# Kernel optimization log

Measured on AMD Instinct MI355X. Metric: run time of the kernel, lower is better.

Reference implementation:

```python
import jax, jax.numpy as jnp
import numpy as np

B, C, H, W = 16, 256, 64, 64
OUT_C = 3
N_TOKENS = 512
N_RES = 3
RED = 4
CB = C // RED  # bottleneck channels in ResChain
DN = ('NCHW', 'OIHW', 'NCHW')


def _conv(x, w, pad):
    return jax.lax.conv_general_dilated(x, w, (1, 1), pad, dimension_numbers=DN)


def setup_inputs() -> dict:
    key = jax.random.key(0)
    ks = jax.random.split(key, 8)
    return {
        'input': jax.random.normal(ks[0], (B, C, H, W), jnp.float32),
        'embed': jax.random.normal(ks[1], (C, N_TOKENS), jnp.float32),  # Quantize codebook [dim, n_embed]
        'res_w1': jax.random.normal(ks[2], (N_RES, CB, C, 3, 3), jnp.float32) * 0.02,
        'res_b1': jnp.zeros((N_RES, CB), jnp.float32),
        'res_w2': jax.random.normal(ks[3], (N_RES, C, CB, 1, 1), jnp.float32) * 0.02,
        'res_b2': jnp.zeros((N_RES, C), jnp.float32),
        'out_w': jax.random.normal(ks[4], (OUT_C, C, 1, 1), jnp.float32) * 0.02,
        'out_b': jnp.zeros((OUT_C,), jnp.float32),
    }


def reference(input, embed, res_w1, res_b1, res_w2, res_b2, out_w, out_b):
    sg = jax.lax.stop_gradient
    # --- Quantize (VQ-VAE codebook lookup, straight-through) ---
    x = jnp.transpose(input, (0, 2, 3, 1))  # [B,H,W,C]
    flat = x.reshape(-1, C)                  # [N, C]
    # squared L2 distance to each code: ||f||^2 - 2 f.e + ||e||^2
    dist = (flat * flat).sum(-1, keepdims=True) - 2.0 * (flat @ embed) + (embed * embed).sum(0)
    idx = jnp.argmin(dist, axis=-1).reshape(B, H, W)        # [B,H,W] int
    quantize = jnp.take(embed.T, idx, axis=0)               # embed_code: [B,H,W,C]
    diff = jnp.mean((sg(quantize) - x) ** 2)
    quantize = x + sg(quantize - x)                         # straight-through
    q = jnp.transpose(quantize, (0, 3, 1, 2))               # [B,C,H,W]
    # --- dec: ResChain(n_res_block) + 1x1 conv ---
    for i in range(N_RES):
        h = jax.nn.relu(q)
        h = _conv(h, res_w1[i], 'SAME') + res_b1[i][None, :, None, None]
        h = jax.nn.relu(h)
        h = _conv(h, res_w2[i], 'VALID') + res_b2[i][None, :, None, None]
        q = q + h
    quant = _conv(q, out_w, 'VALID') + out_b[None, :, None, None]  # [B,OUT_C,H,W]
    # --- wordfreq: per-batch bincount over idx (no grad) ---
    flat_idx = idx.reshape(B, -1)
    seg = (flat_idx + jnp.arange(B, dtype=flat_idx.dtype)[:, None] * N_TOKENS).reshape(-1)
    counts = jax.ops.segment_sum(jnp.ones_like(seg, jnp.float32), seg, num_segments=B * N_TOKENS)
    wordfreq = counts.reshape(B, N_TOKENS) / float(H * W)
    return quant, diff.reshape(1), wordfreq
```

## Files before the change

### kernel.cpp

```cpp
#include <hip/hip_runtime.h>


typedef __attribute__((ext_vector_type(8))) short short8;
typedef __attribute__((ext_vector_type(16))) float f32x16;
typedef __attribute__((ext_vector_type(8))) _Float16 half8;
typedef __attribute__((ext_vector_type(2))) _Float16 half2_t;
typedef unsigned short ushort_t;
typedef unsigned long long u64;

#define WS_QA    0
#define WS_QB    8388608
#define WS_ET    16777216
#define WS_EN    16842752
#define WS_EPK   16843264
#define WS_W1PK  16908800
#define WS_W2PK  17129984
#define WS_DIFF  17154560
#define WS_TOK   17154568
#define WS_DST   17220104
#define WS_FN    17285640
#define WS_WL    17351176

#define MARGIN 0.12f

__device__ inline ushort_t f2bf(float f) {
  unsigned u = __float_as_uint(f);
  return (ushort_t)((u + 0x7fffu + ((u >> 16) & 1u)) >> 16);
}
__device__ inline float bf2f(ushort_t h) { return __uint_as_float(((unsigned)h) << 16); }
union HU { _Float16 h; ushort_t u; };
union S8H { short8 s; half8 h; half2_t h2[4]; };

__global__ __launch_bounds__(256) void prep_kernel(
    const float* __restrict__ embed, const float* __restrict__ w1,
    const float* __restrict__ w2, float* __restrict__ ws, float* __restrict__ wf) {
  int i = blockIdx.x * 256 + threadIdx.x;
  if (i < 131072) {
    int t = i >> 8, c = i & 255;
    ((ushort_t*)(ws + WS_ET))[i] = f2bf(embed[c * 512 + t]);
  }
  if (i < 512) {
    float s = 0.f;
    for (int c = 0; c < 256; ++c) { float v = embed[c * 512 + i]; s += v * v; }
    ws[WS_EN + i] = s;
  }
  if (i < 131072) {
    int j = i & 7, lane = (i >> 3) & 63, at = (i >> 9) & 15, ks = i >> 13;
    int code = at * 32 + (lane & 31);
    int c = ks * 16 + (lane >> 5) * 8 + j;
    HU cv; cv.h = (_Float16)embed[c * 512 + code];
    ((ushort_t*)(ws + WS_EPK))[i] = cv.u;
  }
  if (i < 442368) {
    int j = i & 7; int lane = (i >> 3) & 63; int of = (i >> 9) & 1;
    int k16 = (i >> 10) & 15; int rest = i >> 14;
    int tap = rest % 9; int layer = rest / 9;
    int oc = of * 32 + (lane & 31);
    int c = k16 * 16 + (lane >> 5) * 8 + j;
    ((ushort_t*)(ws + WS_W1PK))[i] = f2bf(w1[((layer * 64 + oc) * 256 + c) * 9 + tap]);
  }
  if (i < 49152) {
    int j = i & 7, lane = (i >> 3) & 63, at = (i >> 9) & 7, ks = (i >> 12) & 3, l = i >> 14;
    int co = at * 32 + (lane & 31), cb = ks * 16 + (lane >> 5) * 8 + j;
    ((ushort_t*)(ws + WS_W2PK))[i] = f2bf(w2[(l * 256 + co) * 64 + cb]);
  }
  if (i < 8192) wf[i] = 0.f;
  if (i == 0) { ws[WS_DIFF] = 0.f; ((int*)(ws + WS_WL))[0] = 0; }
}

__global__ __launch_bounds__(512, 4) void dist_kernel(
    const float* __restrict__ input, const half8* __restrict__ epk,
    const float* __restrict__ enorm, int* __restrict__ tok,
    float* __restrict__ dst, float* __restrict__ fnv, int* __restrict__ wl) {
  __shared__ __align__(16) ushort_t sfp[2048 * 8];
  __shared__ float senorm[512];
  __shared__ float trim1[512], trim2[512];
  __shared__ int   trii[512];

  int blk = blockIdx.x, b = blk >> 6, hw0 = (blk & 63) << 6;
  int tid = threadIdx.x, lane = tid & 63, wave = tid >> 6;
  senorm[tid] = enorm[tid];

  {
    int cg = tid >> 3, sub = tid & 7;
    int ks_s = cg >> 2, hi_s = (cg >> 1) & 1, jq = cg & 1;
    const float* src0 = input + ((size_t)(b * 256 + cg * 4)) * 4096 + hw0 + sub * 8;
    float vv[4][8];
#pragma unroll
    for (int m = 0; m < 4; ++m) {
      const float4* s4 = (const float4*)(src0 + (size_t)m * 4096);
      float4 aa = s4[0], bb = s4[1];
      vv[m][0] = aa.x; vv[m][1] = aa.y; vv[m][2] = aa.z; vv[m][3] = aa.w;
      vv[m][4] = bb.x; vv[m][5] = bb.y; vv[m][6] = bb.z; vv[m][7] = bb.w;
    }
    u64* sfp64 = (u64*)sfp;
#pragma unroll
    for (int i = 0; i < 8; ++i) {
      int pl = sub * 8 + i;
      int bt = pl >> 5, lw = (pl & 31) + 32 * hi_s;
      u64 pk = 0;
#pragma unroll
      for (int m = 0; m < 4; ++m) {
        HU cv; cv.h = (_Float16)vv[m][i];
        pk |= ((u64)cv.u) << (16 * m);
      }
      sfp64[((bt * 16 + ks_s) * 64 + lw) * 2 + jq] = pk;
    }
  }
  __syncthreads();

  f32x16 acc[2][2];
#pragma unroll
  for (int bt = 0; bt < 2; ++bt)
#pragma unroll
    for (int a = 0; a < 2; ++a)
#pragma unroll
      for (int r = 0; r < 16; ++r) acc[bt][a][r] = 0.f;

  const short8* sfp8 = (const short8*)sfp;
  float fnp0 = 0.f, fnp1 = 0.f;
#pragma unroll 2
  for (int ks = 0; ks < 16; ++ks) {
    S8H u0, u1;
    u0.s = sfp8[ks * 64 + lane];
    u1.s = sfp8[(16 + ks) * 64 + lane];
#if __has_builtin(__builtin_amdgcn_fdot2)
#pragma unroll
    for (int k = 0; k < 4; ++k) {
      fnp0 = __builtin_amdgcn_fdot2(u0.h2[k], u0.h2[k], fnp0, false);
      fnp1 = __builtin_amdgcn_fdot2(u1.h2[k], u1.h2[k], fnp1, false);
    }
#else
#pragma unroll
    for (int k = 0; k < 8; ++k) {
      float v0 = (float)u0.h[k], v1 = (float)u1.h[k];
      fnp0 += v0 * v0; fnp1 += v1 * v1;
    }
#endif
#pragma unroll
    for (int a = 0; a < 2; ++a) {
      half8 ah = epk[(ks * 16 + wave * 2 + a) * 64 + lane];
      acc[0][a] = __builtin_amdgcn_mfma_f32_32x32x16_f16(ah, u0.h, acc[0][a], 0, 0, 0);
      acc[1][a] = __builtin_amdgcn_mfma_f32_32x32x16_f16(ah, u1.h, acc[1][a], 0, 0, 0);
    }
  }
  fnp0 += __shfl_xor(fnp0, 32, 64);
  fnp1 += __shfl_xor(fnp1, 32, 64);

  int hi5 = lane >> 5;
#pragma unroll
  for (int bt = 0; bt < 2; ++bt) {
    float m1 = 3.4e38f, m2 = 3.4e38f; int i1 = 0;
#pragma unroll
    for (int a = 0; a < 2; ++a)
#pragma unroll
      for (int r = 0; r < 16; ++r) {
        int code = (wave * 2 + a) * 32 + (r & 3) + 8 * (r >> 2) + 4 * hi5;
        float v = senorm[code] - 2.0f * acc[bt][a][r];
        if (v < m1) { m2 = m1; m1 = v; i1 = code; }
        else if (v < m2) m2 = v;
      }
    float o1 = __shfl_xor(m1, 32, 64);
    float o2 = __shfl_xor(m2, 32, 64);
    int   oi = __shfl_xor(i1, 32, 64);
    float n2 = fminf(fmaxf(m1, o1), fminf(m2, o2));
    float n1 = fminf(m1, o1);
    int   ni = (o1 < m1) ? oi : i1;
    if (lane < 32) {
      int p = bt * 32 + lane;
      trim1[p * 8 + wave] = n1; trim2[p * 8 + wave] = n2; trii[p * 8 + wave] = ni;
    }
  }
  __syncthreads();

  if (wave == 0) {
    int p = lane;
    float m1 = trim1[p * 8], m2 = trim2[p * 8]; int i1 = trii[p * 8];
#pragma unroll
    for (int w = 1; w < 8; ++w) {
      float a1 = trim1[p * 8 + w], a2 = trim2[p * 8 + w]; int ai = trii[p * 8 + w];
      float n2 = fminf(fmaxf(m1, a1), fminf(m2, a2));
      if (a1 < m1) { m1 = a1; i1 = ai; }
      m2 = n2;
    }
    float myfn = (lane < 32) ? fnp0 : fnp1;
    int gpos = blk * 64 + p;
    tok[gpos] = i1;
    dst[gpos] = myfn + m1;
    fnv[gpos] = myfn;
    bool flag = (m2 - m1 < MARGIN);
    u64 mk = __ballot(flag);
    int base = 0;
    if (lane == 0 && mk) base = atomicAdd(wl, (int)__popcll(mk));
    base = __shfl(base, 0, 64);
    if (flag) {
      int off = (int)__popcll(mk & ((1ull << lane) - 1ull));
      wl[1 + base + off] = gpos;
    }
  }
}

__global__ __launch_bounds__(256) void redo_kernel(
    const float* __restrict__ input, const float* __restrict__ embed,
    const float* __restrict__ enorm, const int* __restrict__ wl,
    int* __restrict__ tok, float* __restrict__ dst, const float* __restrict__ fnv) {
  __shared__ float sf[256], rv[256];
  __shared__ int   ri[256];
  int n = wl[0];
  int tid = threadIdx.x;
  for (int e = blockIdx.x; e < n; e += gridDim.x) {
    int gpos = wl[1 + e];
    int b = gpos >> 12, hw = gpos & 4095;
    sf[tid] = input[((size_t)(b * 256 + tid)) * 4096 + hw];
    __syncthreads();
    float d0 = 0.f, d1 = 0.f;
#pragma unroll 4
    for (int c = 0; c < 256; ++c) {
      float fv = sf[c];
      d0 += fv * embed[c * 512 + tid];
      d1 += fv * embed[c * 512 + 256 + tid];
    }
    float v0 = enorm[tid] - 2.f * d0;
    float v1 = enorm[256 + tid] - 2.f * d1;
    float bv; int bi;
    if (v1 < v0) { bv = v1; bi = 256 + tid; } else { bv = v0; bi = tid; }
    rv[tid] = bv; ri[tid] = bi;
    __syncthreads();
    for (int s = 128; s > 0; s >>= 1) {
      if (tid < s) {
        float ov = rv[tid + s]; int oi2 = ri[tid + s];
        if (ov < rv[tid] || (ov == rv[tid] && oi2 < ri[tid])) { rv[tid] = ov; ri[tid] = oi2; }
      }
      __syncthreads();
    }
    if (tid == 0) { tok[gpos] = ri[0]; dst[gpos] = fnv[gpos] + rv[0]; }
    __syncthreads();
  }
}

__global__ __launch_bounds__(256) void finalize_kernel(
    const int* __restrict__ tok, const float* __restrict__ dst,
    const ushort_t* __restrict__ embedT, float* __restrict__ wf,
    float* __restrict__ diffp, ushort_t* __restrict__ qout) {
  int blk = blockIdx.x;
  int tid = threadIdx.x, lane = tid & 63, wave = tid >> 6;
  int gbase = blk * 64;
  int b = gbase >> 12;
  if (wave == 0) {
    int t = tok[gbase + lane];
    atomicAdd(&wf[b * 512 + t], 1.0f / 4096.0f);
    float d = dst[gbase + lane];
#pragma unroll
    for (int off = 32; off >= 1; off >>= 1) d += __shfl_down(d, off, 64);
    if (lane == 0) atomicAdd(diffp, d);
  }
#pragma unroll 1
  for (int j = 0; j < 16; ++j) {
    int p = wave * 16 + j;
    int t = __builtin_amdgcn_readfirstlane(tok[gbase + p]);
    const u64* src = (const u64*)(embedT + (size_t)t * 256);
    u64* dstp = (u64*)(qout + ((size_t)(gbase + p)) * 256);
    dstp[lane] = src[lane];
  }
}

__global__ __launch_bounds__(256, 3) void fused_layer(
    const ushort_t* __restrict__ qin, ushort_t* __restrict__ qout,
    const ushort_t* __restrict__ w1pk, const float* __restrict__ b1,
    const ushort_t* __restrict__ w2pk, const float* __restrict__ b2, int l) {
  __shared__ __align__(16) char arena[42496];
  short8*   stg    = (short8*)arena;
  ushort_t* qstage = (ushort_t*)arena;
  ushort_t* hbuf   = (ushort_t*)(arena + 23040);
  float*    sb2    = (float*)(arena + 41472);

  int blk = blockIdx.x;
  int b = blk >> 5; int t = blk & 31;
  int ty0 = (t >> 2) << 3;
  int tx0 = (t & 3) << 4;
  int tid = threadIdx.x, lane = tid & 63, w = tid >> 6;
  int pt = w >> 1, ot = w & 1;
  int l31 = lane & 31, kb5 = lane >> 5;

  sb2[tid] = b2[l * 256 + tid];

  const short8* wp  = (const short8*)w1pk + (size_t)l * 18432;
  const short8* w2p = (const short8*)w2pk;

  short8 sreg[6];
  auto loadch = [&](int cs) {
#pragma unroll
    for (int s = 0; s < 6; ++s) {
      int u = s * 256 + tid;
      if (u < 1440) {
        int xx = u % 18; int r = u / 18; int cg = r & 7; int yy = r >> 3;
        int sy = ty0 + yy - 1, sx = tx0 + xx - 1;
        if (sy >= 0 && sy < 64 && sx >= 0 && sx < 64) {
          sreg[s] = *(const short8*)(qin + ((size_t)(b * 4096 + sy * 64 + sx)) * 256 + cs * 64 + cg * 8);
        } else {
          short8 z;
#pragma unroll
          for (int k2 = 0; k2 < 8; ++k2) z[k2] = 0;
          sreg[s] = z;
        }
      }
    }
  };
  auto writech = [&]() {
#pragma unroll
    for (int s = 0; s < 6; ++s) {
      int u = s * 256 + tid;
      if (u < 1440) {
        short8 sv = sreg[s];
#pragma unroll
        for (int k2 = 0; k2 < 8; ++k2) if (sv[k2] < 0) sv[k2] = 0;
        stg[u] = sv;
      }
    }
  };

  f32x16 acc[2];
#pragma unroll
  for (int mi = 0; mi < 2; ++mi)
#pragma unroll
    for (int r = 0; r < 16; ++r) acc[mi][r] = 0.f;

  int y0 = pt * 4 + (l31 >> 4);
  int x0 = l31 & 15;

  loadch(0);
  writech();
  __syncthreads();
#pragma unroll 1
  for (int cs = 0; cs < 4; ++cs) {
    if (cs < 3) loadch(cs + 1);
#pragma unroll 1
    for (int dy = 0; dy < 3; ++dy) {
#pragma unroll 1
      for (int dx = 0; dx < 3; ++dx) {
        int tap = dy * 3 + dx;
#pragma unroll
        for (int kk = 0; kk < 4; ++kk) {
          int base = ((y0 + dy) * 8 + kk * 2 + kb5) * 18 + (x0 + dx);
          short8 A0 = stg[base];
          short8 A1 = stg[base + 288];
          short8 B = wp[(tap * 16 + cs * 4 + kk) * 128 + ot * 64 + lane];
          acc[0] = __builtin_amdgcn_mfma_f32_32x32x16_bf16(A0, B, acc[0], 0, 0, 0);
          acc[1] = __builtin_amdgcn_mfma_f32_32x32x16_bf16(A1, B, acc[1], 0, 0, 0);
        }
      }
    }
    __syncthreads();
    if (cs < 3) { writech(); __syncthreads(); }
  }

  {
    int oc = ot * 32 + l31;
    float bb = b1[l * 64 + oc];
#pragma unroll
    for (int mi = 0; mi < 2; ++mi)
#pragma unroll
      for (int r = 0; r < 16; ++r) {
        int row = (r & 3) + 8 * (r >> 2) + 4 * kb5;
        int px = (2 * pt + mi) * 32 + row;
        hbuf[px * 72 + oc] = f2bf(fmaxf(acc[mi][r] + bb, 0.f));
      }
  }
  __syncthreads();

  int pt2 = w >> 1, coh = w & 1;
#pragma unroll 1
  for (int cq = 0; cq < 4; ++cq) {
    short8 qv[4];
#pragma unroll
    for (int it = 0; it < 4; ++it) {
      int u = it * 256 + tid;
      int px = u >> 3, c8 = u & 7;
      int gy = ty0 + (px >> 4), gx = tx0 + (px & 15);
      qv[it] = *(const short8*)(qin + ((size_t)(b * 4096 + gy * 64 + gx)) * 256 + cq * 64 + c8 * 8);
    }

    f32x16 a2[2];
#pragma unroll
    for (int mi = 0; mi < 2; ++mi)
#pragma unroll
      for (int r = 0; r < 16; ++r) a2[mi][r] = 0.f;

#pragma unroll
    for (int ks = 0; ks < 4; ++ks) {
      short8 Bw = w2p[((l * 4 + ks) * 8 + cq * 2 + coh) * 64 + lane];
#pragma unroll
      for (int mi = 0; mi < 2; ++mi) {
        short8 A = *(const short8*)(hbuf + ((2 * pt2 + mi) * 32 + l31) * 72 + ks * 16 + kb5 * 8);
        a2[mi] = __builtin_amdgcn_mfma_f32_32x32x16_bf16(A, Bw, a2[mi], 0, 0, 0);
      }
    }
    {
      int cc = coh * 32 + l31;
      float bb2 = sb2[cq * 64 + cc];
#pragma unroll
      for (int mi = 0; mi < 2; ++mi)
#pragma unroll
        for (int r = 0; r < 16; ++r) {
          int row = (r & 3) + 8 * (r >> 2) + 4 * kb5;
          int px = (2 * pt2 + mi) * 32 + row;
          qstage[px * 72 + cc] = f2bf(a2[mi][r] + bb2);
        }
    }
    __syncthreads();
#pragma unroll
    for (int it = 0; it < 4; ++it) {
      int u = it * 256 + tid;
      int px = u >> 3, c8 = u & 7;
      short8 hv = *(const short8*)(qstage + px * 72 + c8 * 8);
      int gy = ty0 + (px >> 4), gx = tx0 + (px & 15);
      size_t gidx = ((size_t)(b * 4096 + gy * 64 + gx)) * 256 + cq * 64 + c8 * 8;
      short8 ov;
#pragma unroll
      for (int k2 = 0; k2 < 8; ++k2)
        ov[k2] = (short)f2bf(bf2f((ushort_t)qv[it][k2]) + bf2f((ushort_t)hv[k2]));
      *(short8*)(qout + gidx) = ov;
    }
    __syncthreads();
  }
}

__global__ __launch_bounds__(256) void final_kernel(
    const ushort_t* __restrict__ qbuf, const float* __restrict__ ow,
    const float* __restrict__ ob, float* __restrict__ out,
    const float* __restrict__ ws) {
  int t = blockIdx.x * 256 + threadIdx.x;
  int pos = t >> 4, c16 = t & 15;
  const ushort_t* qp = qbuf + (size_t)pos * 256 + c16 * 16;
  short8 v0 = *(const short8*)qp;
  short8 v1 = *(const short8*)(qp + 8);
  float a0 = 0.f, a1 = 0.f, a2 = 0.f;
#pragma unroll
  for (int k = 0; k < 16; ++k) {
    float f = bf2f((ushort_t)(k < 8 ? v0[k] : v1[k - 8]));
    int c = c16 * 16 + k;
    a0 += f * ow[c];
    a1 += f * ow[256 + c];
    a2 += f * ow[512 + c];
  }
#pragma unroll
  for (int off = 1; off < 16; off <<= 1) {
    a0 += __shfl_xor(a0, off, 64);
    a1 += __shfl_xor(a1, off, 64);
    a2 += __shfl_xor(a2, off, 64);
  }
  if (c16 == 0) {
    int b = pos >> 12, hw = pos & 4095;
    out[(b * 3 + 0) * 4096 + hw] = a0 + ob[0];
    out[(b * 3 + 1) * 4096 + hw] = a1 + ob[1];
    out[(b * 3 + 2) * 4096 + hw] = a2 + ob[2];
  }
  if (t == 0) out[196608] = ws[WS_DIFF] * (1.0f / 16777216.0f);
}

extern "C" void kernel_launch(void* const* d_in, const int* in_sizes, int n_in,
                              void* d_out, int out_size, void* d_ws, size_t ws_size,
                              hipStream_t stream) {
  (void)in_sizes; (void)n_in; (void)out_size; (void)ws_size;
  const float* input = (const float*)d_in[0];
  const float* embed = (const float*)d_in[1];
  const float* b1 = (const float*)d_in[3];
  const float* b2 = (const float*)d_in[5];
  const float* ow = (const float*)d_in[6];
  const float* ob = (const float*)d_in[7];
  float* ws = (float*)d_ws;
  float* out = (float*)d_out;
  float* wf = out + 196609;

  ushort_t* qA = (ushort_t*)(ws + WS_QA);
  ushort_t* qB = (ushort_t*)(ws + WS_QB);
  const ushort_t* et = (const ushort_t*)(ws + WS_ET);
  const half8* epk = (const half8*)(ws + WS_EPK);
  const ushort_t* w1pk = (const ushort_t*)(ws + WS_W1PK);
  const ushort_t* w2pk = (const ushort_t*)(ws + WS_W2PK);
  int*   tok = (int*)(ws + WS_TOK);
  float* dst = ws + WS_DST;
  float* fnv = ws + WS_FN;
  int*   wl  = (int*)(ws + WS_WL);

  hipLaunchKernelGGL(prep_kernel, dim3(1728), dim3(256), 0, stream,
                     embed, (const float*)d_in[2], (const float*)d_in[4], ws, wf);
  hipLaunchKernelGGL(dist_kernel, dim3(1024), dim3(512), 0, stream,
                     input, epk, ws + WS_EN, tok, dst, fnv, wl);
  hipLaunchKernelGGL(redo_kernel, dim3(1024), dim3(256), 0, stream,
                     input, embed, ws + WS_EN, wl, tok, dst, fnv);
  hipLaunchKernelGGL(finalize_kernel, dim3(1024), dim3(256), 0, stream,
                     tok, dst, et, wf, ws + WS_DIFF, qA);
  hipLaunchKernelGGL(fused_layer, dim3(512), dim3(256), 0, stream,
                     qA, qB, w1pk, b1, w2pk, b2, 0);
  hipLaunchKernelGGL(fused_layer, dim3(512), dim3(256), 0, stream,
                     qB, qA, w1pk, b1, w2pk, b2, 1);
  hipLaunchKernelGGL(fused_layer, dim3(512), dim3(256), 0, stream,
                     qA, qB, w1pk, b1, w2pk, b2, 2);
  hipLaunchKernelGGL(final_kernel, dim3(4096), dim3(256), 0, stream,
                     qB, ow, ob, out, ws);
}
```

Before: 236.0 us.

## Enlarge fused residual tile to 16x16 with split-K waves and double-buffered staging

The fused residual layer now processes 16x16 pixel tiles with 512-thread blocks, half the previous block count. The 3x3 conv K dimension is split across two wave groups that are reduced through shared memory. Input channel slices of 32 are double-buffered to remove one barrier per slice, and staging addresses are precomputed. The goal is to cut halo reloads and weight fetches per output and to raise MFMA work per A/B load. The costs are a larger LDS footprint (about 80KB), lower occupancy, only 256 blocks across the CUs, and an extra reduction pass.

```diff
diff --git a/kernel.cpp b/kernel.cpp
--- a/kernel.cpp
+++ b/kernel.cpp
@@ -264,156 +264,183 @@
   }
 }
 
-__global__ __launch_bounds__(256, 3) void fused_layer(
+__global__ __launch_bounds__(512, 2) void fused_layer(
     const ushort_t* __restrict__ qin, ushort_t* __restrict__ qout,
     const ushort_t* __restrict__ w1pk, const float* __restrict__ b1,
     const ushort_t* __restrict__ w2pk, const float* __restrict__ b2, int l) {
-  __shared__ __align__(16) char arena[42496];
+  __shared__ __align__(16) char arena[81664];
   short8*   stg    = (short8*)arena;
+  float*    red    = (float*)arena;
   ushort_t* qstage = (ushort_t*)arena;
-  ushort_t* hbuf   = (ushort_t*)(arena + 23040);
-  float*    sb2    = (float*)(arena + 41472);
+  ushort_t* hbuf   = (ushort_t*)(arena + 43776);
+  float*    sb2    = (float*)(arena + 80640);
 
   int blk = blockIdx.x;
-  int b = blk >> 5; int t = blk & 31;
-  int ty0 = (t >> 2) << 3;
+  int b = blk >> 4; int t = blk & 15;
+  int ty0 = (t >> 2) << 4;
   int tx0 = (t & 3) << 4;
   int tid = threadIdx.x, lane = tid & 63, w = tid >> 6;
-  int pt = w >> 1, ot = w & 1;
+  int pq = w & 3, kh = w >> 2;
   int l31 = lane & 31, kb5 = lane >> 5;
 
-  sb2[tid] = b2[l * 256 + tid];
+  if (tid < 256) sb2[tid] = b2[l * 256 + tid];
 
   const short8* wp  = (const short8*)w1pk + (size_t)l * 18432;
   const short8* w2p = (const short8*)w2pk;
 
-  short8 sreg[6];
+  int s_u[3]; size_t s_src[3]; bool s_live[3], s_in[3];
+#pragma unroll
+  for (int s = 0; s < 3; ++s) {
+    int u = s * 512 + tid;
+    bool live = (u < 1368);
+    int cg = 0, yy = 0, xx = 0;
+    if (live) { cg = u / 342; int rem = u - cg * 342; yy = rem / 19; xx = rem - yy * 19; }
+    live = live && (xx < 18);
+    int sy = ty0 + yy - 1, sx = tx0 + xx - 1;
+    bool inb = live && sy >= 0 && sy < 64 && sx >= 0 && sx < 64;
+    s_u[s] = u; s_live[s] = live; s_in[s] = inb;
+    s_src[s] = ((size_t)(b * 4096 + (inb ? sy * 64 + sx : 0))) * 256 + cg * 8;
+  }
+
+  short8 sreg[3];
   auto loadch = [&](int cs) {
 #pragma unroll
-    for (int s = 0; s < 6; ++s) {
-      int u = s * 256 + tid;
-      if (u < 1440) {
-        int xx = u % 18; int r = u / 18; int cg = r & 7; int yy = r >> 3;
-        int sy = ty0 + yy - 1, sx = tx0 + xx - 1;
-        if (sy >= 0 && sy < 64 && sx >= 0 && sx < 64) {
-          sreg[s] = *(const short8*)(qin + ((size_t)(b * 4096 + sy * 64 + sx)) * 256 + cs * 64 + cg * 8);
-        } else {
-          short8 z;
-#pragma unroll
-          for (int k2 = 0; k2 < 8; ++k2) z[k2] = 0;
-          sreg[s] = z;
-        }
+    for (int s = 0; s < 3; ++s) {
+      if (s_live[s]) {
+        if (s_in[s]) sreg[s] = *(const short8*)(qin + s_src[s] + cs * 32);
+        else { short8 z; for (int k2 = 0; k2 < 8; ++k2) z[k2] = 0; sreg[s] = z; }
       }
     }
   };
-  auto writech = [&]() {
-#pragma unroll
-    for (int s = 0; s < 6; ++s) {
-      int u = s * 256 + tid;
-      if (u < 1440) {
+  auto writech = [&](int buf) {
+#pragma unroll
+    for (int s = 0; s < 3; ++s) {
+      if (s_live[s]) {
         short8 sv = sreg[s];
 #pragma unroll
         for (int k2 = 0; k2 < 8; ++k2) if (sv[k2] < 0) sv[k2] = 0;
-        stg[u] = sv;
+        stg[buf * 1368 + s_u[s]] = sv;
       }
     }
   };
 
-  f32x16 acc[2];
+  f32x16 acc[2][2];
 #pragma unroll
   for (int mi = 0; mi < 2; ++mi)
 #pragma unroll
-    for (int r = 0; r < 16; ++r) acc[mi][r] = 0.f;
-
-  int y0 = pt * 4 + (l31 >> 4);
+    for (int nj = 0; nj < 2; ++nj)
+#pragma unroll
+      for (int r = 0; r < 16; ++r) acc[mi][nj][r] = 0.f;
+
+  int ybase = pq * 4 + ((l31 >> 4) & 1);
   int x0 = l31 & 15;
+  int cgA = kh * 2 + kb5;
 
   loadch(0);
-  writech();
-  __syncthreads();
+  writech(0);
 #pragma unroll 1
-  for (int cs = 0; cs < 4; ++cs) {
-    if (cs < 3) loadch(cs + 1);
+  for (int cs = 0; cs < 8; ++cs) {
+    __syncthreads();
+    if (cs < 7) loadch(cs + 1);
+    const short8* sb = stg + (cs & 1) * 1368 + cgA * 342;
+    const short8* wrowb = wp + (size_t)(cs * 2 + kh) * 128 + lane;
 #pragma unroll 1
     for (int dy = 0; dy < 3; ++dy) {
 #pragma unroll 1
       for (int dx = 0; dx < 3; ++dx) {
-        int tap = dy * 3 + dx;
-#pragma unroll
-        for (int kk = 0; kk < 4; ++kk) {
-          int base = ((y0 + dy) * 8 + kk * 2 + kb5) * 18 + (x0 + dx);
-          short8 A0 = stg[base];
-          short8 A1 = stg[base + 288];
-          short8 B = wp[(tap * 16 + cs * 4 + kk) * 128 + ot * 64 + lane];
-          acc[0] = __builtin_amdgcn_mfma_f32_32x32x16_bf16(A0, B, acc[0], 0, 0, 0);
-          acc[1] = __builtin_amdgcn_mfma_f32_32x32x16_bf16(A1, B, acc[1], 0, 0, 0);
+        int a0 = (ybase + dy) * 19 + x0 + dx;
+        short8 A0 = sb[a0];
+        short8 A1 = sb[a0 + 38];
+        const short8* wr = wrowb + (size_t)(dy * 3 + dx) * 16 * 128;
+        short8 B0 = wr[0];
+        short8 B1 = wr[64];
+        acc[0][0] = __builtin_amdgcn_mfma_f32_32x32x16_bf16(A0, B0, acc[0][0], 0, 0, 0);
+        acc[0][1] = __builtin_amdgcn_mfma_f32_32x32x16_bf16(A0, B1, acc[0][1], 0, 0, 0);
+        acc[1][0] = __builtin_amdgcn_mfma_f32_32x32x16_bf16(A1, B0, acc[1][0], 0, 0, 0);
+        acc[1][1] = __builtin_amdgcn_mfma_f32_32x32x16_bf16(A1, B1, acc[1][1], 0, 0, 0);
+      }
+    }
+    if (cs < 7) writech((cs + 1) & 1);
+  }
+  __syncthreads();
+
+#pragma unroll 1
+  for (int mi = 0; mi < 2; ++mi) {
+    if (kh == 1) {
+      float* d = red + (size_t)(pq * 64 + lane) * 33;
+#pragma unroll
+      for (int nj = 0; nj < 2; ++nj)
+#pragma unroll
+        for (int r4 = 0; r4 < 4; ++r4) {
+          float4 v; v.x = acc[mi][nj][r4 * 4]; v.y = acc[mi][nj][r4 * 4 + 1];
+          v.z = acc[mi][nj][r4 * 4 + 2]; v.w = acc[mi][nj][r4 * 4 + 3];
+          *(float4*)(d + nj * 16 + r4 * 4) = v;
         }
-      }
     }
     __syncthreads();
-    if (cs < 3) { writech(); __syncthreads(); }
-  }
-
-  {
-    int oc = ot * 32 + l31;
-    float bb = b1[l * 64 + oc];
-#pragma unroll
-    for (int mi = 0; mi < 2; ++mi)
-#pragma unroll
-      for (int r = 0; r < 16; ++r) {
-        int row = (r & 3) + 8 * (r >> 2) + 4 * kb5;
-        int px = (2 * pt + mi) * 32 + row;
-        hbuf[px * 72 + oc] = f2bf(fmaxf(acc[mi][r] + bb, 0.f));
-      }
-  }
-  __syncthreads();
-
-  int pt2 = w >> 1, coh = w & 1;
+    if (kh == 0) {
+      const float* s = red + (size_t)(pq * 64 + lane) * 33;
+#pragma unroll
+      for (int nj = 0; nj < 2; ++nj) {
+        int oc = nj * 32 + l31;
+        float bb = b1[l * 64 + oc];
+#pragma unroll
+        for (int r = 0; r < 16; ++r) {
+          int row = (r & 3) + 8 * (r >> 2) + 4 * kb5;
+          int px = (pq * 4 + mi * 2 + (row >> 4)) * 16 + (row & 15);
+          hbuf[px * 72 + oc] = f2bf(fmaxf(acc[mi][nj][r] + s[nj * 16 + r] + bb, 0.f));
+        }
+      }
+    }
+    __syncthreads();
+  }
+
+  int coh = kh;
+  int rowb = pq * 64 + coh * 32;
 #pragma unroll 1
   for (int cq = 0; cq < 4; ++cq) {
     short8 qv[4];
 #pragma unroll
     for (int it = 0; it < 4; ++it) {
-      int u = it * 256 + tid;
+      int u = it * 64 + lane;
       int px = u >> 3, c8 = u & 7;
-      int gy = ty0 + (px >> 4), gx = tx0 + (px & 15);
+      int pos = rowb + px;
+      int gy = ty0 + (pos >> 4), gx = tx0 + (pos & 15);
       qv[it] = *(const short8*)(qin + ((size_t)(b * 4096 + gy * 64 + gx)) * 256 + cq * 64 + c8 * 8);
     }
 
     f32x16 a2[2];
 #pragma unroll
-    for (int mi = 0; mi < 2; ++mi)
-#pragma unroll
-      for (int r = 0; r < 16; ++r) a2[mi][r] = 0.f;
+    for (int nj = 0; nj < 2; ++nj)
+#pragma unroll
+      for (int r = 0; r < 16; ++r) a2[nj][r] = 0.f;
 
 #pragma unroll
     for (int ks = 0; ks < 4; ++ks) {
-      short8 Bw = w2p[((l * 4 + ks) * 8 + cq * 2 + coh) * 64 + lane];
-#pragma unroll
-      for (int mi = 0; mi < 2; ++mi) {
-        short8 A = *(const short8*)(hbuf + ((2 * pt2 + mi) * 32 + l31) * 72 + ks * 16 + kb5 * 8);
-        a2[mi] = __builtin_amdgcn_mfma_f32_32x32x16_bf16(A, Bw, a2[mi], 0, 0, 0);
-      }
-    }
-    {
-      int cc = coh * 32 + l31;
+      short8 A = *(const short8*)(hbuf + (rowb + l31) * 72 + ks * 16 + kb5 * 8);
+#pragma unroll
+      for (int nj = 0; nj < 2; ++nj) {
+        short8 B = w2p[((l * 4 + ks) * 8 + cq * 2 + nj) * 64 + lane];
+        a2[nj] = __builtin_amdgcn_mfma_f32_32x32x16_bf16(A, B, a2[nj], 0, 0, 0);
+      }
+    }
+#pragma unroll
+    for (int nj = 0; nj < 2; ++nj) {
+      int cc = nj * 32 + l31;
       float bb2 = sb2[cq * 64 + cc];
 #pragma unroll
-      for (int mi = 0; mi < 2; ++mi)
-#pragma unroll
-        for (int r = 0; r < 16; ++r) {
-          int row = (r & 3) + 8 * (r >> 2) + 4 * kb5;
-          int px = (2 * pt2 + mi) * 32 + row;
-          qstage[px * 72 + cc] = f2bf(a2[mi][r] + bb2);
-        }
-    }
-    __syncthreads();
+      for (int r = 0; r < 16; ++r) {
+        int row = (r & 3) + 8 * (r >> 2) + 4 * kb5;
+        qstage[(rowb + row) * 72 + cc] = f2bf(a2[nj][r] + bb2);
+      }
+    }
 #pragma unroll
     for (int it = 0; it < 4; ++it) {
-      int u = it * 256 + tid;
+      int u = it * 64 + lane;
       int px = u >> 3, c8 = u & 7;
-      short8 hv = *(const short8*)(qstage + px * 72 + c8 * 8);
-      int gy = ty0 + (px >> 4), gx = tx0 + (px & 15);
+      int pos = rowb + px;
+      short8 hv = *(const short8*)(qstage + pos * 72 + c8 * 8);
+      int gy = ty0 + (pos >> 4), gx = tx0 + (pos & 15);
       size_t gidx = ((size_t)(b * 4096 + gy * 64 + gx)) * 256 + cq * 64 + c8 * 8;
       short8 ov;
 #pragma unroll
@@ -421,7 +448,6 @@
         ov[k2] = (short)f2bf(bf2f((ushort_t)qv[it][k2]) + bf2f((ushort_t)hv[k2]));
       *(short8*)(qout + gidx) = ov;
     }
-    __syncthreads();
   }
 }
 
@@ -491,11 +517,11 @@
                      input, embed, ws + WS_EN, wl, tok, dst, fnv);
   hipLaunchKernelGGL(finalize_kernel, dim3(1024), dim3(256), 0, stream,
                      tok, dst, et, wf, ws + WS_DIFF, qA);
-  hipLaunchKernelGGL(fused_layer, dim3(512), dim3(256), 0, stream,
+  hipLaunchKernelGGL(fused_layer, dim3(256), dim3(512), 0, stream,
                      qA, qB, w1pk, b1, w2pk, b2, 0);
-  hipLaunchKernelGGL(fused_layer, dim3(512), dim3(256), 0, stream,
+  hipLaunchKernelGGL(fused_layer, dim3(256), dim3(512), 0, stream,
                      qB, qA, w1pk, b1, w2pk, b2, 1);
-  hipLaunchKernelGGL(fused_layer, dim3(512), dim3(256), 0, stream,
+  hipLaunchKernelGGL(fused_layer, dim3(256), dim3(512), 0, stream,
                      qA, qB, w1pk, b1, w2pk, b2, 2);
   hipLaunchKernelGGL(final_kernel, dim3(4096), dim3(256), 0, stream,
                      qB, ow, ob, out, ws);
```

Result: slower. 389.9 us (+65.2%).
